# Kernel tuning notes

Hardware: AMD Instinct MI355X
Metric: run time of the kernel (lower is better)

Reference implementation:

```python
import jax, jax.numpy as jnp
import numpy as np

NUM_HEADS = 8
SIZE_Q = 512
SIZE_K = 512
SIZE_V = 512
B, S = 2, 2048


def setup_inputs() -> dict:
    key = jax.random.key(0)
    ks = jax.random.split(key, 16)
    Hk = SIZE_K  # num_heads * head_size_k
    Hv = SIZE_V  # num_heads * head_size_v
    inp = {
        "k": jax.random.normal(ks[0], (B, S, SIZE_K), jnp.float32),
        "v": jax.random.normal(ks[1], (B, S, SIZE_V), jnp.float32),
        "q": jax.random.normal(ks[2], (B, S, SIZE_Q), jnp.float32),
        "mask": jax.random.randint(ks[3], (S, S), 0, 2).astype(jnp.bool_),
        "spatial_bias": jax.random.normal(ks[4], (1, NUM_HEADS, S, S), jnp.float32),
        # Linear params stored as [in, out]; y = x @ W + b
        "Wq": jax.random.normal(ks[5], (SIZE_Q, Hk), jnp.float32) / np.sqrt(SIZE_Q),
        "bq": jnp.zeros((Hk,), jnp.float32),
        "Wk": jax.random.normal(ks[6], (SIZE_K, Hk), jnp.float32) / np.sqrt(SIZE_K),
        "bk": jnp.zeros((Hk,), jnp.float32),
        "Wv": jax.random.normal(ks[7], (SIZE_V, Hv), jnp.float32) / np.sqrt(SIZE_V),
        "bv": jnp.zeros((Hv,), jnp.float32),
        "Wo": jax.random.normal(ks[8], (Hv, SIZE_V), jnp.float32) / np.sqrt(Hv),
        "bo": jnp.zeros((SIZE_V,), jnp.float32),
    }
    return inp


def reference(k, v, q, mask, spatial_bias, Wq, bq, Wk, bk, Wv, bv, Wo, bo):
    batch, sk = k.shape[0], k.shape[1]
    sq = q.shape[1]
    hdk = Wk.shape[1] // NUM_HEADS
    hdv = Wv.shape[1] // NUM_HEADS
    # QKV projections -> [B, H, S, hd]
    kp = (k @ Wk + bk).reshape(batch, sk, NUM_HEADS, hdk).transpose(0, 2, 1, 3)
    vp = (v @ Wv + bv).reshape(batch, sk, NUM_HEADS, hdv).transpose(0, 2, 1, 3)
    qp = (q @ Wq + bq).reshape(batch, sq, NUM_HEADS, hdk).transpose(0, 2, 1, 3)
    qp = qp / jnp.sqrt(jnp.asarray(hdk, qp.dtype))
    # Scores with additive spatial bias and boolean mask (2D mask -> [1,1,S,S])
    scores = jnp.einsum("bhqd,bhkd->bhqk", qp, kp) + spatial_bias
    scores = jnp.where(mask[None, None, :, :], scores, -jnp.inf)
    attn = jax.nn.softmax(scores, axis=-1)  # dropout=0 (eval)
    ctx = jnp.einsum("bhqk,bhkd->bhqd", attn, vp)
    ctx = ctx.transpose(0, 2, 1, 3).reshape(batch, sq, NUM_HEADS * hdv)
    return ctx @ Wo + bo
```

## Files before the change

### kernel.cpp

```cpp
#include <hip/hip_runtime.h>
#include <hip/hip_bf16.h>

#define S_LEN 2048
#define NH 8
#define HD 64
#define CH 512
#define NEG_BIG (-3.0e38f)
#define KHALF 1024
#define CTXP_STRIDE (2 * NH * S_LEN * HD)
#define ML_STRIDE   (2 * NH * S_LEN)

typedef __bf16 bf16;
typedef bf16 bf16x8 __attribute__((ext_vector_type(8)));
typedef bf16 bf16x4 __attribute__((ext_vector_type(4)));
typedef float floatx4 __attribute__((ext_vector_type(4)));

typedef const unsigned int __attribute__((address_space(1)))* gas1_t;
typedef unsigned int __attribute__((address_space(3)))* las3_t;
__device__ __forceinline__ void gll16(const void* g, void* l) {
    __builtin_amdgcn_global_load_lds((gas1_t)g, (las3_t)l, 16, 0, 0);
}

__global__ void detect_mask_kernel(const unsigned char* __restrict__ mb,
                                   int* __restrict__ flag_out) {
    __shared__ int s1, s3;
    if (threadIdx.x == 0) { s1 = 0; s3 = 0; }
    __syncthreads();
    int any1 = 0, any3 = 0;
    int base = threadIdx.x * 16;
    for (int i = base; i < base + 16; ++i) {
        unsigned char bch = mb[i];
        int m = i & 3;
        if (bch != 0) {
            if (m == 1) any1 = 1;
            if (m == 2 || m == 3) any3 = 1;
        }
    }
    if (any1) atomicOr(&s1, 1);
    if (any3) atomicOr(&s3, 1);
    __syncthreads();
    if (threadIdx.x == 0) {
        int f = 0;
        if (s1) f = 1;
        else if (s3) f = 2;
        *flag_out = f;
    }
}

__global__ __launch_bounds__(256) void prep_weights_kernel(
    const float* __restrict__ Wq, const float* __restrict__ Wk,
    const float* __restrict__ Wv, const float* __restrict__ Wo,
    bf16* __restrict__ WThi, bf16* __restrict__ WTlo)
{
    __shared__ float tile[64][65];
    const int t = threadIdx.x;
    const int n0 = blockIdx.x * 64;
    const int k0 = blockIdx.y * 64;
    const int mat = blockIdx.z;
    const float* W = (mat == 0) ? Wq : (mat == 1) ? Wk : (mat == 2) ? Wv : Wo;
    bf16* hi = WThi + (size_t)mat * (CH * CH);
    bf16* lo = WTlo + (size_t)mat * (CH * CH);
#pragma unroll
    for (int i = 0; i < 4; ++i) {
        int row = (t >> 4) + 16 * i;
        int c4 = (t & 15) << 2;
        float4 f = *(const float4*)(W + (size_t)(k0 + row) * CH + n0 + c4);
        tile[row][c4 + 0] = f.x; tile[row][c4 + 1] = f.y;
        tile[row][c4 + 2] = f.z; tile[row][c4 + 3] = f.w;
    }
    __syncthreads();
#pragma unroll
    for (int i = 0; i < 4; ++i) {
        int nr = (t >> 4) + 16 * i;
        int k4 = (t & 15) << 2;
        bf16x4 h, l;
#pragma unroll
        for (int j = 0; j < 4; ++j) {
            float x = tile[k4 + j][nr];
            bf16 hv = (bf16)x;
            h[j] = hv;
            l[j] = (bf16)(x - (float)hv);
        }
        *(bf16x4*)(hi + (size_t)(n0 + nr) * CH + k0 + k4) = h;
        *(bf16x4*)(lo + (size_t)(n0 + nr) * CH + k0 + k4) = l;
    }
}

__device__ __forceinline__ void gemm_bf16_tile(
    bf16* __restrict__ As_hi, bf16* __restrict__ As_lo,
    bf16* __restrict__ Bs_hi, bf16* __restrict__ Bs_lo,
    const float* __restrict__ IN, const bf16* __restrict__ WThi,
    const bf16* __restrict__ WTlo, const float* __restrict__ BI,
    float* __restrict__ OUT, bf16* __restrict__ OBF,
    const float* __restrict__ ML, float scale, int mode)
{
    const int t = threadIdx.x;
    const int w = t >> 6;
    const int lane = t & 63;
    const int m16 = lane & 15;
    const int quad = lane >> 4;
    const int m0 = blockIdx.y * 128;
    const int n0 = blockIdx.x * 128;

    const int arow = t >> 1;
    const int akc  = (t & 1) << 4;

    floatx4 acc[2][8];
#pragma unroll
    for (int mi = 0; mi < 2; ++mi)
#pragma unroll
        for (int ni = 0; ni < 8; ++ni) {
            acc[mi][ni][0] = 0.f; acc[mi][ni][1] = 0.f;
            acc[mi][ni][2] = 0.f; acc[mi][ni][3] = 0.f;
        }

    float4 af[4];
    bf16x8 pbh[2], pbl[2];

    auto loadA = [&](int k0) {
        if (ML) {
            int col = k0 + akc;
            int hh = col >> 6, dd = col & 63;
            int row = m0 + arow;
            int bb = row >> 11, ss = row & (S_LEN - 1);
            size_t prow = ((size_t)bb * NH + hh) * S_LEN + ss;
            float m0v = ML[prow * 2],                 l0v = ML[prow * 2 + 1];
            float m1v = ML[(ML_STRIDE + prow) * 2],   l1v = ML[(ML_STRIDE + prow) * 2 + 1];
            float mx = fmaxf(m0v, m1v);
            float e0 = __expf(m0v - mx), e1 = __expf(m1v - mx);
            float den = e0 * l0v + e1 * l1v;
            float inv = den > 0.f ? 1.f / den : 0.f;
            float a0 = e0 * inv, a1 = e1 * inv;
            const float* p0 = IN + prow * HD + dd;
            const float* p1 = p0 + CTXP_STRIDE;
#pragma unroll
            for (int j = 0; j < 4; ++j) {
                float4 c0 = ((const float4*)p0)[j];
                float4 c1 = ((const float4*)p1)[j];
                af[j].x = a0 * c0.x + a1 * c1.x;
                af[j].y = a0 * c0.y + a1 * c1.y;
                af[j].z = a0 * c0.z + a1 * c1.z;
                af[j].w = a0 * c0.w + a1 * c1.w;
            }
        } else {
            const float* p = IN + (size_t)(m0 + arow) * CH + k0 + akc;
            af[0] = ((const float4*)p)[0];
            af[1] = ((const float4*)p)[1];
            af[2] = ((const float4*)p)[2];
            af[3] = ((const float4*)p)[3];
        }
    };
    auto loadB = [&](int k0) {
        const bf16* ph = WThi + (size_t)(n0 + arow) * CH + k0 + akc;
        const bf16* pl = WTlo + (size_t)(n0 + arow) * CH + k0 + akc;
        pbh[0] = ((const bf16x8*)ph)[0]; pbh[1] = ((const bf16x8*)ph)[1];
        pbl[0] = ((const bf16x8*)pl)[0]; pbl[1] = ((const bf16x8*)pl)[1];
    };
    auto stage = [&]() {
#pragma unroll
        for (int hh = 0; hh < 2; ++hh) {
            bf16x8 h, l;
#pragma unroll
            for (int j = 0; j < 8; ++j) {
                float x = ((const float*)&af[2 * hh])[j];
                bf16 hv = (bf16)x;
                h[j] = hv;
                l[j] = (bf16)(x - (float)hv);
            }
            *(bf16x8*)&As_hi[arow * 40 + akc + 8 * hh] = h;
            *(bf16x8*)&As_lo[arow * 40 + akc + 8 * hh] = l;
        }
        *(bf16x8*)&Bs_hi[arow * 40 + akc + 0] = pbh[0];
        *(bf16x8*)&Bs_hi[arow * 40 + akc + 8] = pbh[1];
        *(bf16x8*)&Bs_lo[arow * 40 + akc + 0] = pbl[0];
        *(bf16x8*)&Bs_lo[arow * 40 + akc + 8] = pbl[1];
    };

    loadA(0); loadB(0);
    for (int ks = 0; ks < CH / 32; ++ks) {
        __syncthreads();
        stage();
        __syncthreads();
        if (ks + 1 < CH / 32) { loadA(32 * (ks + 1)); loadB(32 * (ks + 1)); }

        bf16x8 bh[8], bl[8];
#pragma unroll
        for (int ni = 0; ni < 8; ++ni) {
            bh[ni] = *(const bf16x8*)&Bs_hi[(16 * ni + m16) * 40 + 8 * quad];
            bl[ni] = *(const bf16x8*)&Bs_lo[(16 * ni + m16) * 40 + 8 * quad];
        }
#pragma unroll
        for (int mi = 0; mi < 2; ++mi) {
            bf16x8 ah = *(const bf16x8*)&As_hi[(32 * w + 16 * mi + m16) * 40 + 8 * quad];
            bf16x8 al = *(const bf16x8*)&As_lo[(32 * w + 16 * mi + m16) * 40 + 8 * quad];
#pragma unroll
            for (int ni = 0; ni < 8; ++ni) {
                acc[mi][ni] = __builtin_amdgcn_mfma_f32_16x16x32_bf16(ah, bh[ni], acc[mi][ni], 0, 0, 0);
                acc[mi][ni] = __builtin_amdgcn_mfma_f32_16x16x32_bf16(ah, bl[ni], acc[mi][ni], 0, 0, 0);
                acc[mi][ni] = __builtin_amdgcn_mfma_f32_16x16x32_bf16(al, bh[ni], acc[mi][ni], 0, 0, 0);
            }
        }
    }

#pragma unroll
    for (int mi = 0; mi < 2; ++mi) {
#pragma unroll
        for (int r = 0; r < 4; ++r) {
            int row = m0 + 32 * w + 16 * mi + 4 * quad + r;
            int bb = row >> 11;
            int ss = row & (S_LEN - 1);
#pragma unroll
            for (int ni = 0; ni < 8; ++ni) {
                int col = n0 + 16 * ni + m16;
                float v = (acc[mi][ni][r] + BI[col]) * scale;
                if (mode == 0) {
                    int hh = col >> 6, dd = col & 63;
                    OUT[(((size_t)bb * NH + hh) * S_LEN + ss) * HD + dd] = v;
                } else if (mode == 3) {
                    int hh = col >> 6, dd = col & 63;
                    OBF[((size_t)(bb * NH + hh) * S_LEN + ss) * HD
                        + (((dd >> 3) ^ (ss & 7)) << 3) + (dd & 7)] = (bf16)v;
                } else if (mode == 4) {
                    int hh = col >> 6, dd = col & 63;
                    OBF[((size_t)(bb * NH + hh) * HD + dd) * S_LEN
                        + (ss & ~63) + ((((ss >> 3) & 7) ^ (dd & 7)) << 3) + (ss & 7)] = (bf16)v;
                } else {
                    OUT[(size_t)row * CH + col] = v;
                }
            }
        }
    }
}

__global__ __launch_bounds__(256, 2) void qkv_gemm_kernel(
    const float* __restrict__ q_in, const float* __restrict__ k_in,
    const float* __restrict__ v_in,
    const bf16* __restrict__ WThi, const bf16* __restrict__ WTlo,
    const float* __restrict__ bq, const float* __restrict__ bk,
    const float* __restrict__ bv,
    float* __restrict__ qp, bf16* __restrict__ kswz, bf16* __restrict__ vswz)
{
    __shared__ __attribute__((aligned(16))) bf16 As_hi[128 * 40];
    __shared__ __attribute__((aligned(16))) bf16 As_lo[128 * 40];
    __shared__ __attribute__((aligned(16))) bf16 Bs_hi[128 * 40];
    __shared__ __attribute__((aligned(16))) bf16 Bs_lo[128 * 40];
    int z = blockIdx.z;
    if (z == 0)
        gemm_bf16_tile(As_hi, As_lo, Bs_hi, Bs_lo, q_in,
                       WThi, WTlo, bq, qp, nullptr, nullptr, 0.125f, 0);
    else if (z == 1)
        gemm_bf16_tile(As_hi, As_lo, Bs_hi, Bs_lo, k_in,
                       WThi + (size_t)CH * CH, WTlo + (size_t)CH * CH, bk,
                       nullptr, kswz, nullptr, 1.0f, 3);
    else
        gemm_bf16_tile(As_hi, As_lo, Bs_hi, Bs_lo, v_in,
                       WThi + (size_t)2 * CH * CH, WTlo + (size_t)2 * CH * CH, bv,
                       nullptr, vswz, nullptr, 1.0f, 4);
}

__global__ __launch_bounds__(256, 2) void out_gemm_kernel(
    const float* __restrict__ ctxp, const float* __restrict__ ml,
    const bf16* __restrict__ WThi, const bf16* __restrict__ WTlo,
    const float* __restrict__ bo, float* __restrict__ out)
{
    __shared__ __attribute__((aligned(16))) bf16 As_hi[128 * 40];
    __shared__ __attribute__((aligned(16))) bf16 As_lo[128 * 40];
    __shared__ __attribute__((aligned(16))) bf16 Bs_hi[128 * 40];
    __shared__ __attribute__((aligned(16))) bf16 Bs_lo[128 * 40];
    gemm_bf16_tile(As_hi, As_lo, Bs_hi, Bs_lo, ctxp,
                   WThi + (size_t)3 * CH * CH, WTlo + (size_t)3 * CH * CH, bo,
                   out, nullptr, ml, 1.0f, 2);
}

__global__ __launch_bounds__(256, 4) void attn_kernel(
    const float* __restrict__ qp, const bf16* __restrict__ kswz,
    const bf16* __restrict__ vswz, const float* __restrict__ bias,
    const void* __restrict__ mask, const int* __restrict__ flagp,
    float* __restrict__ ctxp, float* __restrict__ ml)
{
    __shared__ __attribute__((aligned(16))) bf16 Kt[2][64 * 64];
    __shared__ __attribute__((aligned(16))) bf16 Vt[2][64 * 64];
    __shared__ __attribute__((aligned(16))) bf16 Pbf[64 * 72];

    const int t    = threadIdx.x;
    const int w    = t >> 6;
    const int lane = t & 63;
    const int m16  = lane & 15;
    const int quad = lane >> 4;
    const int mx7  = m16 & 7;

    const int p  = blockIdx.x + 32 * (blockIdx.y + 8 * blockIdx.z);
    const int l  = (p & 7) * 128 + (p >> 3);
    const int b  = l & 1;
    const int kz = (l >> 1) & 1;
    const int h  = (l >> 2) & 7;
    const int qi = l >> 5;

    const int q0   = qi * 64;
    const int bh   = b * NH + h;
    const int flag = *flagp;
    const int kbeg = kz * KHALF;

    bf16x8 qf[2];
    {
        const float* qrow =
            qp + ((size_t)bh * S_LEN + q0 + 16 * w + m16) * HD + 8 * quad;
#pragma unroll
        for (int c = 0; c < 2; ++c) {
            float4 f0 = *(const float4*)(qrow + 32 * c);
            float4 f1 = *(const float4*)(qrow + 32 * c + 4);
            bf16x8 v;
            v[0] = (bf16)f0.x; v[1] = (bf16)f0.y; v[2] = (bf16)f0.z; v[3] = (bf16)f0.w;
            v[4] = (bf16)f1.x; v[5] = (bf16)f1.y; v[6] = (bf16)f1.z; v[7] = (bf16)f1.w;
            qf[c] = v;
        }
    }

    floatx4 ctxa[4];
    float mrow[4], lrow[4];
#pragma unroll
    for (int tt = 0; tt < 4; ++tt) { ctxa[tt][0]=0.f; ctxa[tt][1]=0.f; ctxa[tt][2]=0.f; ctxa[tt][3]=0.f; }
#pragma unroll
    for (int r = 0; r < 4; ++r) { mrow[r] = NEG_BIG; lrow[r] = 0.f; }

    const int qrow0 = q0 + 16 * w + 4 * quad;
    const float* bbase = bias + ((size_t)h * S_LEN + qrow0) * S_LEN + m16;
    const unsigned char* mb8  = (const unsigned char*)mask + (size_t)qrow0 * S_LEN + m16;
    const unsigned int*  mb32 = (const unsigned int*)mask  + (size_t)qrow0 * S_LEN + m16;

    float bnext[16]; unsigned mnext[16]; float mb[16];
    auto prefetchBM = [&](int k0) {
        if (flag == 1) {
#pragma unroll
            for (int r = 0; r < 4; ++r)
#pragma unroll
                for (int tt = 0; tt < 4; ++tt)
                    mnext[4 * r + tt] = mb8[(size_t)r * S_LEN + k0 + 16 * tt];
        } else {
#pragma unroll
            for (int r = 0; r < 4; ++r)
#pragma unroll
                for (int tt = 0; tt < 4; ++tt)
                    mnext[4 * r + tt] = mb32[(size_t)r * S_LEN + k0 + 16 * tt];
        }
#pragma unroll
        for (int r = 0; r < 4; ++r)
#pragma unroll
            for (int tt = 0; tt < 4; ++tt)
                bnext[4 * r + tt] = bbase[(size_t)r * S_LEN + k0 + 16 * tt];
    };

    const bf16* kb = kswz + (size_t)bh * S_LEN * HD;
    const bf16* vb = vswz + (size_t)bh * HD * S_LEN;
    const int lrow8 = lane >> 3;
    const int lcol8 = (lane & 7) * 8;

    auto stageKV = [&](int k0, int buf) {
#pragma unroll
        for (int i = 0; i < 2; ++i) {
            int c = 2 * w + i;
            int row = 8 * c + lrow8;
            gll16(kb + (size_t)(k0 + row) * HD + lcol8, &Kt[buf][c * 512]);
            gll16(vb + (size_t)row * S_LEN + k0 + lcol8, &Vt[buf][c * 512]);
        }
    };

    prefetchBM(kbeg);
    stageKV(kbeg, 0);
    __syncthreads();
    int cur = 0;

    for (int k0 = kbeg; k0 < kbeg + KHALF; k0 += 64) {
        const bool more = (k0 + 64 < kbeg + KHALF);
        if (more) stageKV(k0 + 64, cur ^ 1);

#pragma unroll
        for (int j = 0; j < 16; ++j) mb[j] = mnext[j] ? bnext[j] : NEG_BIG;
        if (more) prefetchBM(k0 + 64);

        const bf16* Kc = Kt[cur];
        const bf16* Vc = Vt[cur];
        floatx4 sc[4];
#pragma unroll
        for (int tt = 0; tt < 4; ++tt) { sc[tt][0]=0.f; sc[tt][1]=0.f; sc[tt][2]=0.f; sc[tt][3]=0.f; }
#pragma unroll
        for (int st = 0; st < 2; ++st)
#pragma unroll
            for (int tt = 0; tt < 4; ++tt) {
                bf16x8 kf = *(const bf16x8*)&Kc[(16 * tt + m16) * 64
                                                + (((quad + 4 * st) ^ mx7) << 3)];
                sc[tt] = __builtin_amdgcn_mfma_f32_16x16x32_bf16(qf[st], kf, sc[tt], 0, 0, 0);
            }

        float alpha[4];
#pragma unroll
        for (int r = 0; r < 4; ++r) {
            int lrowq = 16 * w + 4 * quad + r;
            float s[4];
#pragma unroll
            for (int tt = 0; tt < 4; ++tt)
                s[tt] = sc[tt][r] + mb[4 * r + tt];
            float mx = fmaxf(fmaxf(s[0], s[1]), fmaxf(s[2], s[3]));
            mx = fmaxf(mx, __shfl_xor(mx, 1));
            mx = fmaxf(mx, __shfl_xor(mx, 2));
            mx = fmaxf(mx, __shfl_xor(mx, 4));
            mx = fmaxf(mx, __shfl_xor(mx, 8));
            float mnew = fmaxf(mrow[r], mx);
            float al = __expf(mrow[r] - mnew);
            float ls = 0.f;
#pragma unroll
            for (int tt = 0; tt < 4; ++tt) {
                float px = (s[tt] <= -1e37f) ? 0.f : __expf(s[tt] - mnew);
                ls += px;
                Pbf[lrowq * 72 + 16 * tt + m16] = (bf16)px;
            }
            ls += __shfl_xor(ls, 1);
            ls += __shfl_xor(ls, 2);
            ls += __shfl_xor(ls, 4);
            ls += __shfl_xor(ls, 8);
            lrow[r] = lrow[r] * al + ls;
            mrow[r] = mnew;
            alpha[r] = al;
        }
#pragma unroll
        for (int tt = 0; tt < 4; ++tt)
#pragma unroll
            for (int r = 0; r < 4; ++r) ctxa[tt][r] *= alpha[r];

#pragma unroll
        for (int st = 0; st < 2; ++st) {
            bf16x8 pf = *(const bf16x8*)&Pbf[(16 * w + m16) * 72 + 8 * quad + 32 * st];
#pragma unroll
            for (int tt = 0; tt < 4; ++tt) {
                bf16x8 vf = *(const bf16x8*)&Vc[(16 * tt + m16) * 64
                                                + (((quad + 4 * st) ^ mx7) << 3)];
                ctxa[tt] = __builtin_amdgcn_mfma_f32_16x16x32_bf16(pf, vf, ctxa[tt], 0, 0, 0);
            }
        }

        __syncthreads();
        cur ^= 1;
    }

    float* cp = ctxp + (size_t)kz * CTXP_STRIDE;
#pragma unroll
    for (int r = 0; r < 4; ++r) {
        int grow = q0 + 16 * w + 4 * quad + r;
        size_t prow = (size_t)bh * S_LEN + grow;
#pragma unroll
        for (int tt = 0; tt < 4; ++tt)
            cp[prow * HD + 16 * tt + m16] = ctxa[tt][r];
        if (m16 == 0) {
            ml[((size_t)kz * ML_STRIDE + prow) * 2 + 0] = mrow[r];
            ml[((size_t)kz * ML_STRIDE + prow) * 2 + 1] = lrow[r];
        }
    }
}

extern "C" void kernel_launch(void* const* d_in, const int* in_sizes, int n_in,
                              void* d_out, int out_size, void* d_ws, size_t ws_size,
                              hipStream_t stream) {
    const float* k_in = (const float*)d_in[0];
    const float* v_in = (const float*)d_in[1];
    const float* q_in = (const float*)d_in[2];
    const void*  mask = d_in[3];
    const float* bias = (const float*)d_in[4];
    const float* Wq = (const float*)d_in[5];
    const float* bq = (const float*)d_in[6];
    const float* Wk = (const float*)d_in[7];
    const float* bk = (const float*)d_in[8];
    const float* Wv = (const float*)d_in[9];
    const float* bv = (const float*)d_in[10];
    const float* Wo = (const float*)d_in[11];
    const float* bo = (const float*)d_in[12];
    float* out = (float*)d_out;

    char* base = (char*)d_ws;
    float* qp   = (float*)(base);
    float* ctxp = (float*)(base + (8u  << 20));
    float* mlb  = (float*)(base + (24u << 20));
    bf16*  kswz = (bf16*)(base + (25u << 20));
    bf16*  vswz = (bf16*)(base + (29u << 20));
    bf16*  WThi = (bf16*)(base + (33u << 20));
    bf16*  WTlo = (bf16*)(base + (35u << 20));
    int*   flag = (int*) (base + (37u << 20));

    detect_mask_kernel<<<1, 256, 0, stream>>>((const unsigned char*)mask, flag);
    prep_weights_kernel<<<dim3(8, 8, 4), 256, 0, stream>>>(
        Wq, Wk, Wv, Wo, WThi, WTlo);
    qkv_gemm_kernel<<<dim3(4, 32, 3), 256, 0, stream>>>(
        q_in, k_in, v_in, WThi, WTlo, bq, bk, bv, qp, kswz, vswz);
    attn_kernel<<<dim3(32, 8, 4), 256, 0, stream>>>(
        qp, kswz, vswz, bias, mask, flag, ctxp, mlb);
    out_gemm_kernel<<<dim3(4, 32, 1), 256, 0, stream>>>(
        ctxp, mlb, WThi, WTlo, bo, out);
}
```

Measured before the change: 358.5 us.

## Split-K the QKV and output GEMMs with atomic accumulation into bias-initialized buffers

Both projection GEMMs now use split-K: the QKV GEMM splits K in two (six z-slices), the output GEMM in four. Partial results are combined with float atomic adds into buffers that a new kernel fills with the biases first. Because K/V can no longer be written directly as swizzled bf16, they go to fp32 scratch and a separate convert kernel produces the swizzled layout. The aim is more blocks for better GPU occupancy, at the cost of atomic traffic, extra fp32 intermediate memory, two extra launches, and non-deterministic summation order.

Measured after the change: 439.4 us. 22.6% more time.

```diff
diff --git a/kernel.cpp b/kernel.cpp
--- a/kernel.cpp
+++ b/kernel.cpp
@@ -86,13 +86,44 @@
     }
 }
 
-__device__ __forceinline__ void gemm_bf16_tile(
+__global__ __launch_bounds__(256) void init_bias_kernel(
+    const float* __restrict__ bq, const float* __restrict__ bk,
+    const float* __restrict__ bv, const float* __restrict__ bo,
+    float* __restrict__ qp, float* __restrict__ kp32,
+    float* __restrict__ vp32T, float* __restrict__ out)
+{
+    int idx = blockIdx.x * 256 + threadIdx.x;
+    int seg = idx >> 19;
+    int i   = idx & 524287;
+    int f   = i << 2;
+    float4 v;
+    if (seg == 0 || seg == 1) {
+        int d = f & 63;
+        int h = (f >> 17) & 7;
+        int col = h * HD + d;
+        v = *(const float4*)((seg == 0 ? bq : bk) + col);
+        if (seg == 0) { v.x *= 0.125f; v.y *= 0.125f; v.z *= 0.125f; v.w *= 0.125f; }
+        ((float4*)(seg == 0 ? qp : kp32))[i] = v;
+    } else if (seg == 2) {
+        int d = (f >> 11) & 63;
+        int h = (f >> 17) & 7;
+        float b = bv[h * HD + d];
+        v.x = b; v.y = b; v.z = b; v.w = b;
+        ((float4*)vp32T)[i] = v;
+    } else {
+        int col = f & (CH - 1);
+        v = *(const float4*)(bo + col);
+        ((float4*)out)[i] = v;
+    }
+}
+
+__device__ __forceinline__ void gemm_splitk_tile(
     bf16* __restrict__ As_hi, bf16* __restrict__ As_lo,
     bf16* __restrict__ Bs_hi, bf16* __restrict__ Bs_lo,
     const float* __restrict__ IN, const bf16* __restrict__ WThi,
-    const bf16* __restrict__ WTlo, const float* __restrict__ BI,
-    float* __restrict__ OUT, bf16* __restrict__ OBF,
-    const float* __restrict__ ML, float scale, int mode)
+    const bf16* __restrict__ WTlo, float* __restrict__ OUT,
+    const float* __restrict__ ML, float scale, int mode,
+    int kbeg, int kiters)
 {
     const int t = threadIdx.x;
     const int w = t >> 6;
@@ -176,12 +207,12 @@
         *(bf16x8*)&Bs_lo[arow * 40 + akc + 8] = pbl[1];
     };
 
-    loadA(0); loadB(0);
-    for (int ks = 0; ks < CH / 32; ++ks) {
+    loadA(kbeg); loadB(kbeg);
+    for (int ks = 0; ks < kiters; ++ks) {
         __syncthreads();
         stage();
         __syncthreads();
-        if (ks + 1 < CH / 32) { loadA(32 * (ks + 1)); loadB(32 * (ks + 1)); }
+        if (ks + 1 < kiters) { loadA(kbeg + 32 * (ks + 1)); loadB(kbeg + 32 * (ks + 1)); }
 
         bf16x8 bh[8], bl[8];
 #pragma unroll
@@ -212,20 +243,15 @@
 #pragma unroll
             for (int ni = 0; ni < 8; ++ni) {
                 int col = n0 + 16 * ni + m16;
-                float v = (acc[mi][ni][r] + BI[col]) * scale;
+                float v = acc[mi][ni][r] * scale;
                 if (mode == 0) {
                     int hh = col >> 6, dd = col & 63;
-                    OUT[(((size_t)bb * NH + hh) * S_LEN + ss) * HD + dd] = v;
-                } else if (mode == 3) {
+                    unsafeAtomicAdd(&OUT[(((size_t)bb * NH + hh) * S_LEN + ss) * HD + dd], v);
+                } else if (mode == 1) {
                     int hh = col >> 6, dd = col & 63;
-                    OBF[((size_t)(bb * NH + hh) * S_LEN + ss) * HD
-                        + (((dd >> 3) ^ (ss & 7)) << 3) + (dd & 7)] = (bf16)v;
-                } else if (mode == 4) {
-                    int hh = col >> 6, dd = col & 63;
-                    OBF[((size_t)(bb * NH + hh) * HD + dd) * S_LEN
-                        + (ss & ~63) + ((((ss >> 3) & 7) ^ (dd & 7)) << 3) + (ss & 7)] = (bf16)v;
+                    unsafeAtomicAdd(&OUT[(((size_t)bb * NH + hh) * HD + dd) * S_LEN + ss], v);
                 } else {
-                    OUT[(size_t)row * CH + col] = v;
+                    unsafeAtomicAdd(&OUT[(size_t)row * CH + col], v);
                 }
             }
         }
@@ -236,40 +262,70 @@
     const float* __restrict__ q_in, const float* __restrict__ k_in,
     const float* __restrict__ v_in,
     const bf16* __restrict__ WThi, const bf16* __restrict__ WTlo,
-    const float* __restrict__ bq, const float* __restrict__ bk,
-    const float* __restrict__ bv,
-    float* __restrict__ qp, bf16* __restrict__ kswz, bf16* __restrict__ vswz)
+    float* __restrict__ qp, float* __restrict__ kp32, float* __restrict__ vp32T)
 {
     __shared__ __attribute__((aligned(16))) bf16 As_hi[128 * 40];
     __shared__ __attribute__((aligned(16))) bf16 As_lo[128 * 40];
     __shared__ __attribute__((aligned(16))) bf16 Bs_hi[128 * 40];
     __shared__ __attribute__((aligned(16))) bf16 Bs_lo[128 * 40];
-    int z = blockIdx.z;
-    if (z == 0)
-        gemm_bf16_tile(As_hi, As_lo, Bs_hi, Bs_lo, q_in,
-                       WThi, WTlo, bq, qp, nullptr, nullptr, 0.125f, 0);
-    else if (z == 1)
-        gemm_bf16_tile(As_hi, As_lo, Bs_hi, Bs_lo, k_in,
-                       WThi + (size_t)CH * CH, WTlo + (size_t)CH * CH, bk,
-                       nullptr, kswz, nullptr, 1.0f, 3);
+    int unit = blockIdx.z >> 1;
+    int kbeg = (blockIdx.z & 1) * 256;
+    if (unit == 0)
+        gemm_splitk_tile(As_hi, As_lo, Bs_hi, Bs_lo, q_in,
+                         WThi, WTlo, qp, nullptr, 0.125f, 0, kbeg, 8);
+    else if (unit == 1)
+        gemm_splitk_tile(As_hi, As_lo, Bs_hi, Bs_lo, k_in,
+                         WThi + (size_t)CH * CH, WTlo + (size_t)CH * CH,
+                         kp32, nullptr, 1.0f, 0, kbeg, 8);
     else
-        gemm_bf16_tile(As_hi, As_lo, Bs_hi, Bs_lo, v_in,
-                       WThi + (size_t)2 * CH * CH, WTlo + (size_t)2 * CH * CH, bv,
-                       nullptr, vswz, nullptr, 1.0f, 4);
+        gemm_splitk_tile(As_hi, As_lo, Bs_hi, Bs_lo, v_in,
+                         WThi + (size_t)2 * CH * CH, WTlo + (size_t)2 * CH * CH,
+                         vp32T, nullptr, 1.0f, 1, kbeg, 8);
 }
 
 __global__ __launch_bounds__(256, 2) void out_gemm_kernel(
     const float* __restrict__ ctxp, const float* __restrict__ ml,
     const bf16* __restrict__ WThi, const bf16* __restrict__ WTlo,
-    const float* __restrict__ bo, float* __restrict__ out)
+    float* __restrict__ out)
 {
     __shared__ __attribute__((aligned(16))) bf16 As_hi[128 * 40];
     __shared__ __attribute__((aligned(16))) bf16 As_lo[128 * 40];
     __shared__ __attribute__((aligned(16))) bf16 Bs_hi[128 * 40];
     __shared__ __attribute__((aligned(16))) bf16 Bs_lo[128 * 40];
-    gemm_bf16_tile(As_hi, As_lo, Bs_hi, Bs_lo, ctxp,
-                   WThi + (size_t)3 * CH * CH, WTlo + (size_t)3 * CH * CH, bo,
-                   out, nullptr, ml, 1.0f, 2);
+    gemm_splitk_tile(As_hi, As_lo, Bs_hi, Bs_lo, ctxp,
+                     WThi + (size_t)3 * CH * CH, WTlo + (size_t)3 * CH * CH,
+                     out, ml, 1.0f, 2, blockIdx.z * 128, 4);
+}
+
+__global__ __launch_bounds__(256) void convert_kernel(
+    const float* __restrict__ kp32, const float* __restrict__ vp32T,
+    bf16* __restrict__ kswz, bf16* __restrict__ vswz)
+{
+    int idx = blockIdx.x * 256 + threadIdx.x;
+    if (blockIdx.z == 0) {
+        int d8 = idx & 7;
+        int s  = (idx >> 3) & (S_LEN - 1);
+        int bh = idx >> 14;
+        const float* p = kp32 + ((size_t)bh * S_LEN + s) * HD + d8 * 8;
+        float4 f0 = ((const float4*)p)[0];
+        float4 f1 = ((const float4*)p)[1];
+        bf16x8 v;
+        v[0]=(bf16)f0.x; v[1]=(bf16)f0.y; v[2]=(bf16)f0.z; v[3]=(bf16)f0.w;
+        v[4]=(bf16)f1.x; v[5]=(bf16)f1.y; v[6]=(bf16)f1.z; v[7]=(bf16)f1.w;
+        *(bf16x8*)(kswz + ((size_t)bh * S_LEN + s) * HD + ((d8 ^ (s & 7)) << 3)) = v;
+    } else {
+        int sg = idx & 255;
+        int d  = (idx >> 8) & (HD - 1);
+        int bh = idx >> 14;
+        const float* p = vp32T + ((size_t)bh * HD + d) * S_LEN + sg * 8;
+        float4 f0 = ((const float4*)p)[0];
+        float4 f1 = ((const float4*)p)[1];
+        bf16x8 v;
+        v[0]=(bf16)f0.x; v[1]=(bf16)f0.y; v[2]=(bf16)f0.z; v[3]=(bf16)f0.w;
+        v[4]=(bf16)f1.x; v[5]=(bf16)f1.y; v[6]=(bf16)f1.z; v[7]=(bf16)f1.w;
+        int og = (sg & ~7) | ((sg & 7) ^ (d & 7));
+        *(bf16x8*)(vswz + ((size_t)bh * HD + d) * S_LEN + og * 8) = v;
+    }
 }
 
 __global__ __launch_bounds__(256, 4) void attn_kernel(
@@ -476,22 +532,28 @@
     float* out = (float*)d_out;
 
     char* base = (char*)d_ws;
-    float* qp   = (float*)(base);
-    float* ctxp = (float*)(base + (8u  << 20));
-    float* mlb  = (float*)(base + (24u << 20));
-    bf16*  kswz = (bf16*)(base + (25u << 20));
-    bf16*  vswz = (bf16*)(base + (29u << 20));
-    bf16*  WThi = (bf16*)(base + (33u << 20));
-    bf16*  WTlo = (bf16*)(base + (35u << 20));
-    int*   flag = (int*) (base + (37u << 20));
+    float* qp    = (float*)(base);
+    float* ctxp  = (float*)(base + (8u  << 20));
+    float* mlb   = (float*)(base + (24u << 20));
+    bf16*  kswz  = (bf16*) (base + (25u << 20));
+    bf16*  vswz  = (bf16*) (base + (29u << 20));
+    bf16*  WThi  = (bf16*) (base + (33u << 20));
+    bf16*  WTlo  = (bf16*) (base + (35u << 20));
+    float* kp32  = (float*)(base + (37u << 20));
+    float* vp32T = (float*)(base + (45u << 20));
+    int*   flag  = (int*)  (base + (53u << 20));
 
     detect_mask_kernel<<<1, 256, 0, stream>>>((const unsigned char*)mask, flag);
     prep_weights_kernel<<<dim3(8, 8, 4), 256, 0, stream>>>(
         Wq, Wk, Wv, Wo, WThi, WTlo);
-    qkv_gemm_kernel<<<dim3(4, 32, 3), 256, 0, stream>>>(
-        q_in, k_in, v_in, WThi, WTlo, bq, bk, bv, qp, kswz, vswz);
+    init_bias_kernel<<<8192, 256, 0, stream>>>(
+        bq, bk, bv, bo, qp, kp32, vp32T, out);
+    qkv_gemm_kernel<<<dim3(4, 32, 6), 256, 0, stream>>>(
+        q_in, k_in, v_in, WThi, WTlo, qp, kp32, vp32T);
+    convert_kernel<<<dim3(1024, 1, 2), 256, 0, stream>>>(
+        kp32, vp32T, kswz, vswz);
     attn_kernel<<<dim3(32, 8, 4), 256, 0, stream>>>(
         qp, kswz, vswz, bias, mask, flag, ctxp, mlb);
-    out_gemm_kernel<<<dim3(4, 32, 1), 256, 0, stream>>>(
-        ctxp, mlb, WThi, WTlo, bo, out);
-}
+    out_gemm_kernel<<<dim3(4, 32, 4), 256, 0, stream>>>(
+        ctxp, mlb, WThi, WTlo, out);
+}
```

## Double-buffer GEMM LDS tiles and split-K the output projection

Applied to the files above, without the earlier changes.

The shared GEMM tile routine now keeps two LDS buffers. It stages the next K-slice while MFMAs run on the current one, which cuts the barriers per iteration from two to one, and it shrinks the row pitch from 40 to 36 elements. The output projection is split along K into two halves across blockIdx.z, doubling its block count from 128 to 256 so more CUs are busy. A new reduction kernel then sums the two partial outputs and adds the bias. This costs an extra 8 MB partial-buffer write and read plus one more launch, and the 36-element pitch may change LDS bank-conflict behaviour.

New measurement: 442.2 us. 1.23x slower.

```diff
diff --git a/kernel.cpp b/kernel.cpp
--- a/kernel.cpp
+++ b/kernel.cpp
@@ -9,6 +9,8 @@
 #define KHALF 1024
 #define CTXP_STRIDE (2 * NH * S_LEN * HD)
 #define ML_STRIDE   (2 * NH * S_LEN)
+#define LDS_T (128 * 36)
+#define OUTP_STRIDE (4096 * 512)
 
 typedef __bf16 bf16;
 typedef bf16 bf16x8 __attribute__((ext_vector_type(8)));
@@ -92,7 +94,8 @@
     const float* __restrict__ IN, const bf16* __restrict__ WThi,
     const bf16* __restrict__ WTlo, const float* __restrict__ BI,
     float* __restrict__ OUT, bf16* __restrict__ OBF,
-    const float* __restrict__ ML, float scale, int mode)
+    const float* __restrict__ ML, float scale, int mode,
+    int kbeg, int kiters)
 {
     const int t = threadIdx.x;
     const int w = t >> 6;
@@ -156,7 +159,8 @@
         pbh[0] = ((const bf16x8*)ph)[0]; pbh[1] = ((const bf16x8*)ph)[1];
         pbl[0] = ((const bf16x8*)pl)[0]; pbl[1] = ((const bf16x8*)pl)[1];
     };
-    auto stage = [&]() {
+    auto stage = [&](int buf) {
+        int base = buf * LDS_T;
 #pragma unroll
         for (int hh = 0; hh < 2; ++hh) {
             bf16x8 h, l;
@@ -167,32 +171,33 @@
                 h[j] = hv;
                 l[j] = (bf16)(x - (float)hv);
             }
-            *(bf16x8*)&As_hi[arow * 40 + akc + 8 * hh] = h;
-            *(bf16x8*)&As_lo[arow * 40 + akc + 8 * hh] = l;
-        }
-        *(bf16x8*)&Bs_hi[arow * 40 + akc + 0] = pbh[0];
-        *(bf16x8*)&Bs_hi[arow * 40 + akc + 8] = pbh[1];
-        *(bf16x8*)&Bs_lo[arow * 40 + akc + 0] = pbl[0];
-        *(bf16x8*)&Bs_lo[arow * 40 + akc + 8] = pbl[1];
+            *(bf16x8*)&As_hi[base + arow * 36 + akc + 8 * hh] = h;
+            *(bf16x8*)&As_lo[base + arow * 36 + akc + 8 * hh] = l;
+        }
+        *(bf16x8*)&Bs_hi[base + arow * 36 + akc + 0] = pbh[0];
+        *(bf16x8*)&Bs_hi[base + arow * 36 + akc + 8] = pbh[1];
+        *(bf16x8*)&Bs_lo[base + arow * 36 + akc + 0] = pbl[0];
+        *(bf16x8*)&Bs_lo[base + arow * 36 + akc + 8] = pbl[1];
     };
 
-    loadA(0); loadB(0);
-    for (int ks = 0; ks < CH / 32; ++ks) {
-        __syncthreads();
-        stage();
-        __syncthreads();
-        if (ks + 1 < CH / 32) { loadA(32 * (ks + 1)); loadB(32 * (ks + 1)); }
-
+    loadA(kbeg); loadB(kbeg);
+    stage(0);
+    if (kiters > 1) { loadA(kbeg + 32); loadB(kbeg + 32); }
+    __syncthreads();
+    int cur = 0;
+
+    for (int ks = 0; ks < kiters; ++ks) {
+        int cb = cur * LDS_T;
         bf16x8 bh[8], bl[8];
 #pragma unroll
         for (int ni = 0; ni < 8; ++ni) {
-            bh[ni] = *(const bf16x8*)&Bs_hi[(16 * ni + m16) * 40 + 8 * quad];
-            bl[ni] = *(const bf16x8*)&Bs_lo[(16 * ni + m16) * 40 + 8 * quad];
+            bh[ni] = *(const bf16x8*)&Bs_hi[cb + (16 * ni + m16) * 36 + 8 * quad];
+            bl[ni] = *(const bf16x8*)&Bs_lo[cb + (16 * ni + m16) * 36 + 8 * quad];
         }
 #pragma unroll
         for (int mi = 0; mi < 2; ++mi) {
-            bf16x8 ah = *(const bf16x8*)&As_hi[(32 * w + 16 * mi + m16) * 40 + 8 * quad];
-            bf16x8 al = *(const bf16x8*)&As_lo[(32 * w + 16 * mi + m16) * 40 + 8 * quad];
+            bf16x8 ah = *(const bf16x8*)&As_hi[cb + (32 * w + 16 * mi + m16) * 36 + 8 * quad];
+            bf16x8 al = *(const bf16x8*)&As_lo[cb + (32 * w + 16 * mi + m16) * 36 + 8 * quad];
 #pragma unroll
             for (int ni = 0; ni < 8; ++ni) {
                 acc[mi][ni] = __builtin_amdgcn_mfma_f32_16x16x32_bf16(ah, bh[ni], acc[mi][ni], 0, 0, 0);
@@ -200,6 +205,12 @@
                 acc[mi][ni] = __builtin_amdgcn_mfma_f32_16x16x32_bf16(al, bh[ni], acc[mi][ni], 0, 0, 0);
             }
         }
+        if (ks + 1 < kiters) {
+            stage(cur ^ 1);
+            if (ks + 2 < kiters) { loadA(kbeg + 32 * (ks + 2)); loadB(kbeg + 32 * (ks + 2)); }
+        }
+        __syncthreads();
+        cur ^= 1;
     }
 
 #pragma unroll
@@ -212,7 +223,8 @@
 #pragma unroll
             for (int ni = 0; ni < 8; ++ni) {
                 int col = n0 + 16 * ni + m16;
-                float v = (acc[mi][ni][r] + BI[col]) * scale;
+                float v = BI ? (acc[mi][ni][r] + BI[col]) * scale
+                             : acc[mi][ni][r] * scale;
                 if (mode == 0) {
                     int hh = col >> 6, dd = col & 63;
                     OUT[(((size_t)bb * NH + hh) * S_LEN + ss) * HD + dd] = v;
@@ -240,36 +252,55 @@
     const float* __restrict__ bv,
     float* __restrict__ qp, bf16* __restrict__ kswz, bf16* __restrict__ vswz)
 {
-    __shared__ __attribute__((aligned(16))) bf16 As_hi[128 * 40];
-    __shared__ __attribute__((aligned(16))) bf16 As_lo[128 * 40];
-    __shared__ __attribute__((aligned(16))) bf16 Bs_hi[128 * 40];
-    __shared__ __attribute__((aligned(16))) bf16 Bs_lo[128 * 40];
+    __shared__ __attribute__((aligned(16))) bf16 As_hi[2 * LDS_T];
+    __shared__ __attribute__((aligned(16))) bf16 As_lo[2 * LDS_T];
+    __shared__ __attribute__((aligned(16))) bf16 Bs_hi[2 * LDS_T];
+    __shared__ __attribute__((aligned(16))) bf16 Bs_lo[2 * LDS_T];
     int z = blockIdx.z;
     if (z == 0)
         gemm_bf16_tile(As_hi, As_lo, Bs_hi, Bs_lo, q_in,
-                       WThi, WTlo, bq, qp, nullptr, nullptr, 0.125f, 0);
+                       WThi, WTlo, bq, qp, nullptr, nullptr, 0.125f, 0, 0, 16);
     else if (z == 1)
         gemm_bf16_tile(As_hi, As_lo, Bs_hi, Bs_lo, k_in,
                        WThi + (size_t)CH * CH, WTlo + (size_t)CH * CH, bk,
-                       nullptr, kswz, nullptr, 1.0f, 3);
+                       nullptr, kswz, nullptr, 1.0f, 3, 0, 16);
     else
         gemm_bf16_tile(As_hi, As_lo, Bs_hi, Bs_lo, v_in,
                        WThi + (size_t)2 * CH * CH, WTlo + (size_t)2 * CH * CH, bv,
-                       nullptr, vswz, nullptr, 1.0f, 4);
+                       nullptr, vswz, nullptr, 1.0f, 4, 0, 16);
 }
 
 __global__ __launch_bounds__(256, 2) void out_gemm_kernel(
     const float* __restrict__ ctxp, const float* __restrict__ ml,
     const bf16* __restrict__ WThi, const bf16* __restrict__ WTlo,
-    const float* __restrict__ bo, float* __restrict__ out)
+    float* __restrict__ outp)
 {
-    __shared__ __attribute__((aligned(16))) bf16 As_hi[128 * 40];
-    __shared__ __attribute__((aligned(16))) bf16 As_lo[128 * 40];
-    __shared__ __attribute__((aligned(16))) bf16 Bs_hi[128 * 40];
-    __shared__ __attribute__((aligned(16))) bf16 Bs_lo[128 * 40];
+    __shared__ __attribute__((aligned(16))) bf16 As_hi[2 * LDS_T];
+    __shared__ __attribute__((aligned(16))) bf16 As_lo[2 * LDS_T];
+    __shared__ __attribute__((aligned(16))) bf16 Bs_hi[2 * LDS_T];
+    __shared__ __attribute__((aligned(16))) bf16 Bs_lo[2 * LDS_T];
+    int z = blockIdx.z;
     gemm_bf16_tile(As_hi, As_lo, Bs_hi, Bs_lo, ctxp,
-                   WThi + (size_t)3 * CH * CH, WTlo + (size_t)3 * CH * CH, bo,
-                   out, nullptr, ml, 1.0f, 2);
+                   WThi + (size_t)3 * CH * CH, WTlo + (size_t)3 * CH * CH,
+                   nullptr, outp + (size_t)z * OUTP_STRIDE, nullptr, ml,
+                   1.0f, 2, z * 256, 8);
+}
+
+__global__ __launch_bounds__(256) void add_out_kernel(
+    const float* __restrict__ outp, const float* __restrict__ bo,
+    float* __restrict__ out)
+{
+    int idx = blockIdx.x * 256 + threadIdx.x;
+    int col4 = (idx & 127) << 2;
+    float4 a = ((const float4*)outp)[idx];
+    float4 b = ((const float4*)(outp + OUTP_STRIDE))[idx];
+    float4 c = *(const float4*)(bo + col4);
+    float4 o;
+    o.x = a.x + b.x + c.x;
+    o.y = a.y + b.y + c.y;
+    o.z = a.z + b.z + c.z;
+    o.w = a.w + b.w + c.w;
+    ((float4*)out)[idx] = o;
 }
 
 __global__ __launch_bounds__(256, 4) void attn_kernel(
@@ -479,11 +510,12 @@
     float* qp   = (float*)(base);
     float* ctxp = (float*)(base + (8u  << 20));
     float* mlb  = (float*)(base + (24u << 20));
-    bf16*  kswz = (bf16*)(base + (25u << 20));
-    bf16*  vswz = (bf16*)(base + (29u << 20));
-    bf16*  WThi = (bf16*)(base + (33u << 20));
-    bf16*  WTlo = (bf16*)(base + (35u << 20));
-    int*   flag = (int*) (base + (37u << 20));
+    bf16*  kswz = (bf16*) (base + (25u << 20));
+    bf16*  vswz = (bf16*) (base + (29u << 20));
+    bf16*  WThi = (bf16*) (base + (33u << 20));
+    bf16*  WTlo = (bf16*) (base + (35u << 20));
+    float* outp = (float*)(base + (37u << 20));
+    int*   flag = (int*)  (base + (53u << 20));
 
     detect_mask_kernel<<<1, 256, 0, stream>>>((const unsigned char*)mask, flag);
     prep_weights_kernel<<<dim3(8, 8, 4), 256, 0, stream>>>(
@@ -492,6 +524,7 @@
         q_in, k_in, v_in, WThi, WTlo, bq, bk, bv, qp, kswz, vswz);
     attn_kernel<<<dim3(32, 8, 4), 256, 0, stream>>>(
         qp, kswz, vswz, bias, mask, flag, ctxp, mlb);
-    out_gemm_kernel<<<dim3(4, 32, 1), 256, 0, stream>>>(
-        ctxp, mlb, WThi, WTlo, bo, out);
-}
+    out_gemm_kernel<<<dim3(4, 32, 2), 256, 0, stream>>>(
+        ctxp, mlb, WThi, WTlo, outp);
+    add_out_kernel<<<2048, 256, 0, stream>>>(outp, bo, out);
+}
```
